# Kernel tuning notes

Measured on AMD Instinct MI355X. Metric: run time of the kernel, lower is better.

Reference implementation:

```python
import jax, jax.numpy as jnp
import numpy as np

N_NODES = 100000
N_EDGES = 1600000
D_IN = 128
D_HID = 128
D_OUT = 2
BN_EPS = 1e-5


def _sage_conv(x, src, dst, W_l, b_l, W_r):
    # PyG SAGEConv (aggr='mean'): out = lin_l(mean_{j in N(i)} x_j) + lin_r(x_i)
    # messages flow src -> dst
    agg = jax.ops.segment_sum(x[src], dst, num_segments=x.shape[0])
    deg = jax.ops.segment_sum(jnp.ones((src.shape[0],), x.dtype), dst,
                              num_segments=x.shape[0])
    mean = agg / jnp.maximum(deg, 1.0)[:, None]
    return mean @ W_l + b_l + x @ W_r


def _batch_norm(x, gamma, beta):
    # training-mode BatchNorm1d math over the node dimension (biased var)
    mu = jnp.mean(x, axis=0)
    var = jnp.var(x, axis=0)
    return (x - mu) * jax.lax.rsqrt(var + BN_EPS) * gamma + beta


def setup_inputs() -> dict:
    key = jax.random.key(0)
    ks = jax.random.split(key, 10)
    s = lambda d: 1.0 / np.sqrt(d)
    x = jax.random.normal(ks[0], (N_NODES, D_IN), dtype=jnp.float32)
    edge_index = jax.random.randint(ks[1], (2, N_EDGES), 0, N_NODES, dtype=jnp.int64)
    W1l = jax.random.uniform(ks[2], (D_IN, D_HID), jnp.float32, -s(D_IN), s(D_IN))
    b1 = jax.random.uniform(ks[3], (D_HID,), jnp.float32, -s(D_IN), s(D_IN))
    W1r = jax.random.uniform(ks[4], (D_IN, D_HID), jnp.float32, -s(D_IN), s(D_IN))
    W2l = jax.random.uniform(ks[5], (D_HID, D_OUT), jnp.float32, -s(D_HID), s(D_HID))
    b2 = jax.random.uniform(ks[6], (D_OUT,), jnp.float32, -s(D_HID), s(D_HID))
    W2r = jax.random.uniform(ks[7], (D_HID, D_OUT), jnp.float32, -s(D_HID), s(D_HID))
    gamma1 = jnp.ones((D_HID,), jnp.float32)
    beta1 = jnp.zeros((D_HID,), jnp.float32)
    gamma2 = jnp.ones((D_OUT,), jnp.float32)
    beta2 = jnp.zeros((D_OUT,), jnp.float32)
    return {"x": x, "edge_index": edge_index,
            "W1l": W1l, "b1": b1, "W1r": W1r, "gamma1": gamma1, "beta1": beta1,
            "W2l": W2l, "b2": b2, "W2r": W2r, "gamma2": gamma2, "beta2": beta2}


def reference(x, edge_index, W1l, b1, W1r, gamma1, beta1,
              W2l, b2, W2r, gamma2, beta2):
    src, dst = edge_index[0], edge_index[1]
    h = _sage_conv(x, src, dst, W1l, b1, W1r)
    h = _batch_norm(h, gamma1, beta1)
    h = jax.nn.relu(h)
    # dropout in eval mode = identity
    h = _sage_conv(h, src, dst, W2l, b2, W2r)
    h = _batch_norm(h, gamma2, beta2)
    return jax.nn.log_softmax(h, axis=1)
```

## Files before the change

### kernel.cpp

```cpp
#include <hip/hip_runtime.h>
#include <hip/hip_bf16.h>
#include <math.h>


#define DH 128
#define PAD 64
#define NPB 128
#define CAPB (NPB * PAD)
#define MAXBINS 1024
#define MAXCHUNK 6400
#define SENT 0xFFFFFFFFu
#define L1BLOCKS 512

typedef short short8 __attribute__((ext_vector_type(8)));
typedef float float4v __attribute__((ext_vector_type(4)));
typedef float float2v __attribute__((ext_vector_type(2)));
typedef unsigned uint4v __attribute__((ext_vector_type(4)));

template <typename T> static __device__ __forceinline__ float tof(T v);
template <> __device__ __forceinline__ float tof<float>(float v) { return v; }
template <> __device__ __forceinline__ float tof<__hip_bfloat16>(__hip_bfloat16 v) {
  return __bfloat162float(v);
}

static __device__ __forceinline__ short f2bf_s(float f) {
  union { __hip_bfloat16 h; short s; } u;
  u.h = __float2bfloat16(f);
  return u.s;
}

static __device__ __forceinline__ float bf2f(short s) {
  union { unsigned u; float f; } c;
  c.u = ((unsigned)(unsigned short)s) << 16;
  return c.f;
}

static __device__ __forceinline__ float asf(unsigned u) {
  union { unsigned u; float f; } c;
  c.u = u;
  return c.f;
}

__global__ void k_probe(const unsigned* __restrict__ xw,
                        const unsigned* __restrict__ ew,
                        int* __restrict__ flags) {
  int t = threadIdx.x;
  unsigned wx = xw[(size_t)t * 23456 + 7];
  unsigned el = (wx >> 7) & 0xFFu;
  int sx = (el >= 0x60 && el <= 0x85) ? 1 : 0;
  unsigned we = ew[(size_t)t * 12000 + 1];
  int se = (we == 0) ? 1 : 0;
  __shared__ int c[2];
  if (t < 2) c[t] = 0;
  __syncthreads();
  atomicAdd(&c[0], sx);
  atomicAdd(&c[1], se);
  __syncthreads();
  if (t == 0) {
    flags[0] = (c[0] < 192) ? 1 : 0;
    flags[2] = (c[1] > 192) ? 1 : 0;
  }
}

template <typename FT>
static __device__ __forceinline__ void wt_one(const FT* __restrict__ W1l,
                                              const FT* __restrict__ W1r,
                                              short* __restrict__ WT, int idx) {
  int n = idx >> 8, k = idx & 255;
  float v = (k < 128) ? tof(W1l[k * 128 + n]) : tof(W1r[(k - 128) * 128 + n]);
  WT[n * 256 + (k ^ ((n & 7) << 3))] = f2bf_s(v);
}
__global__ void k_xbwt(const void* __restrict__ x, const void* __restrict__ W1l,
                       const void* __restrict__ W1r, const int* __restrict__ flags,
                       __hip_bfloat162* __restrict__ xb, short* __restrict__ WT,
                       int total2) {
  int gi = blockIdx.x * blockDim.x + threadIdx.x;
  bool f32 = flags[0] != 0;
  if (gi < 32768) {
    if (f32) wt_one<float>((const float*)W1l, (const float*)W1r, WT, gi);
    else wt_one<__hip_bfloat16>((const __hip_bfloat16*)W1l, (const __hip_bfloat16*)W1r, WT, gi);
  }
  int i = gi - 32768;
  if (i >= 0 && i < total2) {
    if (f32) {
      float2 v = ((const float2*)x)[i];
      __hip_bfloat162 o;
      o.x = __float2bfloat16(v.x);
      o.y = __float2bfloat16(v.y);
      xb[i] = o;
    } else {
      xb[i] = ((const __hip_bfloat162*)x)[i];
    }
  }
}

template <typename IT>
static __device__ __forceinline__ void binscatter_agg_body(
    const IT* __restrict__ es, const IT* __restrict__ ed,
    int* __restrict__ binCnt, unsigned* __restrict__ pairs,
    int E, int N, int chunk, int NB) {
  __shared__ int cnt[MAXBINS];
  __shared__ int sc[MAXBINS];
  __shared__ int gbase[MAXBINS];
  __shared__ unsigned buf[MAXCHUNK];
  int t = threadIdx.x;
  int e0 = blockIdx.x * chunk;
  int e1 = min(e0 + chunk, E);
  int nE = e1 - e0;
  if (nE <= 0) return;

  for (int b = t; b < MAXBINS; b += 256) cnt[b] = 0;
  __syncthreads();
  for (int i = t; i < nE; i += 256) {
    int d = (int)ed[e0 + i];
    if ((unsigned)d >= (unsigned)N) d = 0;
    atomicAdd(&cnt[d >> 7], 1);
  }
  __syncthreads();
  for (int b = t; b < MAXBINS; b += 256) sc[b] = cnt[b];
  __syncthreads();
  for (int off = 1; off < MAXBINS; off <<= 1) {
    int v[MAXBINS / 256];
#pragma unroll
    for (int j = 0; j < MAXBINS / 256; ++j) {
      int b = t + j * 256;
      v[j] = (b >= off) ? sc[b - off] : 0;
    }
    __syncthreads();
#pragma unroll
    for (int j = 0; j < MAXBINS / 256; ++j) sc[t + j * 256] += v[j];
    __syncthreads();
  }
  for (int b = t; b < NB; b += 256) {
    int c = cnt[b];
    sc[b] -= c;
    int g = 0;
    if (c > 0) g = atomicAdd(&binCnt[b * 16], c);
    gbase[b] = g;
    cnt[b] = 0;
  }
  __syncthreads();
  for (int i = t; i < nE; i += 256) {
    int s = (int)es[e0 + i], d = (int)ed[e0 + i];
    if ((unsigned)s >= (unsigned)N) s = 0;
    if ((unsigned)d >= (unsigned)N) d = 0;
    int bin = d >> 7;
    int p = atomicAdd(&cnt[bin], 1);
    buf[sc[bin] + p] = ((unsigned)(d & (NPB - 1)) << 20) | (unsigned)s;
  }
  __syncthreads();
  for (int b = t; b < NB; b += 256) {
    int c = cnt[b];
    if (c == 0) continue;
    int g = gbase[b];
    if (g >= CAPB) continue;
    int cv = min(c, CAPB - g);
    unsigned* dst = pairs + (size_t)b * CAPB + g;
    const unsigned* srcp = buf + sc[b];
    for (int j = 0; j < cv; ++j) dst[j] = srcp[j];
  }
}
__launch_bounds__(256)
__global__ void k_binscatter_agg(const void* __restrict__ ev, const int* __restrict__ flags,
                                 int* __restrict__ binCnt, unsigned* __restrict__ pairs,
                                 int E, int N, int chunk, int NB) {
  if (flags[2]) binscatter_agg_body<long long>((const long long*)ev, (const long long*)ev + E,
                                               binCnt, pairs, E, N, chunk, NB);
  else          binscatter_agg_body<int>((const int*)ev, (const int*)ev + E,
                                         binCnt, pairs, E, N, chunk, NB);
}

__launch_bounds__(256)
__global__ void k_binbuild(const unsigned* __restrict__ pairs,
                           const int* __restrict__ binCnt,
                           int* __restrict__ deg_i, int* __restrict__ srcs_pad, int N) {
  __shared__ int cnt[NPB];
  __shared__ int lst[NPB * PAD];
  int bin = blockIdx.x;
  int t = threadIdx.x;
  for (int i = t; i < NPB; i += 256) cnt[i] = 0;
  for (int i = t; i < NPB * PAD; i += 256) lst[i] = 0;
  __syncthreads();
  int m = min(binCnt[bin * 16], CAPB);
  const unsigned* pp = pairs + (size_t)bin * CAPB;
  for (int i = t; i < m; i += 256) {
    unsigned u = pp[i];
    if (u == SENT) continue;
    int local = u >> 20;
    int s = u & 0xFFFFF;
    int r = atomicAdd(&cnt[local], 1);
    if (r < PAD) lst[local * PAD + r] = s;
  }
  __syncthreads();
  int base = bin * NPB;
  for (int i = t; i < NPB; i += 256) {
    int node = base + i;
    if (node < N) deg_i[node] = cnt[i];
  }
  for (int i = t; i < NPB * PAD; i += 256) {
    int node = base + (i >> 6);
    if (node < N) srcs_pad[(size_t)base * PAD + i] = lst[i];
  }
}

static __device__ __forceinline__ void accum8(float2v acc[4], uint4v u) {
#pragma unroll
  for (int i = 0; i < 4; ++i) {
    float2v p;
    p[0] = asf(u[i] << 16);
    p[1] = asf(u[i] & 0xFFFF0000u);
    acc[i] += p;
  }
}
static __device__ __forceinline__ uint4v maskv(uint4v v, int keep) {
  unsigned m = keep ? 0xFFFFFFFFu : 0u;
  uint4v r;
#pragma unroll
  for (int i = 0; i < 4; ++i) r[i] = v[i] & m;
  return r;
}
__launch_bounds__(256)
__global__ void k_gather(const unsigned* __restrict__ xbu,
                         const int* __restrict__ deg_i, const int* __restrict__ srcs_pad,
                         short* __restrict__ meanbs, int N) {
  int node = blockIdx.x * 4 + (threadIdx.x >> 6);
  int lane = threadIdx.x & 63;
  int g = lane >> 4, l = lane & 15;
  if (node >= N) return;
  int dg = deg_i[node];
  int cnt = min(dg, PAD);
  const int* sl = srcs_pad + (size_t)node * PAD;
  int srcv = sl[lane];
  const uint4v* xv = (const uint4v*)xbu;
  float2v acc[4];
#pragma unroll
  for (int i = 0; i < 4; ++i) acc[i] = (float2v){0.f, 0.f};

  if (cnt > 0) {
    int sA0 = __shfl(srcv, g);
    int sA1 = __shfl(srcv, 4 + g);
    int sA2 = __shfl(srcv, 8 + g);
    int sA3 = __shfl(srcv, 12 + g);
    uint4v a0 = xv[(size_t)sA0 * 16 + l];
    uint4v a1 = xv[(size_t)sA1 * 16 + l];
    uint4v a2 = xv[(size_t)sA2 * 16 + l];
    uint4v a3 = xv[(size_t)sA3 * 16 + l];
    uint4v b0, b1, b2, b3;
    bool hb = cnt > 16;
    if (hb) {
      int sB0 = __shfl(srcv, 16 + g);
      int sB1 = __shfl(srcv, 20 + g);
      int sB2 = __shfl(srcv, 24 + g);
      int sB3 = __shfl(srcv, 28 + g);
      b0 = xv[(size_t)sB0 * 16 + l];
      b1 = xv[(size_t)sB1 * 16 + l];
      b2 = xv[(size_t)sB2 * 16 + l];
      b3 = xv[(size_t)sB3 * 16 + l];
    }
    a0 = maskv(a0, g < cnt);
    a1 = maskv(a1, 4 + g < cnt);
    a2 = maskv(a2, 8 + g < cnt);
    a3 = maskv(a3, 12 + g < cnt);
    accum8(acc, a0);
    accum8(acc, a1);
    accum8(acc, a2);
    accum8(acc, a3);
    if (hb) {
      b0 = maskv(b0, 16 + g < cnt);
      b1 = maskv(b1, 20 + g < cnt);
      b2 = maskv(b2, 24 + g < cnt);
      b3 = maskv(b3, 28 + g < cnt);
      accum8(acc, b0);
      accum8(acc, b1);
      accum8(acc, b2);
      accum8(acc, b3);
    }
    for (int j = 32; j < cnt; j += 16) {
      int s0 = __shfl(srcv, j + g);
      int s1 = __shfl(srcv, j + 4 + g);
      int s2 = __shfl(srcv, j + 8 + g);
      int s3 = __shfl(srcv, j + 12 + g);
      uint4v v0 = xv[(size_t)s0 * 16 + l];
      uint4v v1 = xv[(size_t)s1 * 16 + l];
      uint4v v2 = xv[(size_t)s2 * 16 + l];
      uint4v v3 = xv[(size_t)s3 * 16 + l];
      v0 = maskv(v0, j + g < cnt);
      v1 = maskv(v1, j + 4 + g < cnt);
      v2 = maskv(v2, j + 8 + g < cnt);
      v3 = maskv(v3, j + 12 + g < cnt);
      accum8(acc, v0);
      accum8(acc, v1);
      accum8(acc, v2);
      accum8(acc, v3);
    }
  }

#pragma unroll
  for (int i = 0; i < 4; ++i) {
#pragma unroll
    for (int c = 0; c < 2; ++c) {
      acc[i][c] += __shfl_xor(acc[i][c], 16);
      acc[i][c] += __shfl_xor(acc[i][c], 32);
    }
  }
  if (g == 0) {
    float invd = 1.0f / fmaxf((float)dg, 1.0f);
    short8 o;
#pragma unroll
    for (int i = 0; i < 4; ++i) {
      o[2 * i]     = f2bf_s(acc[i][0] * invd);
      o[2 * i + 1] = f2bf_s(acc[i][1] * invd);
    }
    *(short8*)(meanbs + (size_t)node * DH + l * 8) = o;
  }
}

template <typename FT>
static __device__ __forceinline__ void layer1_body(
    const short* __restrict__ meanbs, const short* __restrict__ xbs,
    const short* __restrict__ WTs, const FT* __restrict__ b1,
    __hip_bfloat16* __restrict__ h1, float* __restrict__ st1,
    int N, int ntiles) {
  __shared__ short ldsWT[32768];
  int t = threadIdx.x;
  {
    const uint4v* src = (const uint4v*)WTs;
    uint4v* dst = (uint4v*)ldsWT;
#pragma unroll
    for (int i = 0; i < 16; ++i) dst[t + i * 256] = src[t + i * 256];
  }
  __syncthreads();

  int w = t >> 6;
  int lane = t & 63;
  int m = lane & 15;
  int quad = lane >> 4;
  int xm = (m & 7) << 3;

  float bs[8], bq[8];
#pragma unroll
  for (int c = 0; c < 8; ++c) { bs[c] = 0.f; bq[c] = 0.f; }
  float bias[8];
#pragma unroll
  for (int c = 0; c < 8; ++c) bias[c] = tof(b1[c * 16 + m]);

  for (int tt = blockIdx.x; tt < ntiles; tt += gridDim.x) {
    int rowbase = tt * 64 + w * 16;
    int arowc = min(rowbase + m, N - 1);

    short8 afrag[8];
    const short* mr = meanbs + (size_t)arowc * DH;
#pragma unroll
    for (int kt = 0; kt < 4; ++kt)
      afrag[kt] = *(const short8*)(mr + kt * 32 + quad * 8);
    const short* xr = xbs + (size_t)arowc * DH;
#pragma unroll
    for (int kt = 0; kt < 4; ++kt)
      afrag[4 + kt] = *(const short8*)(xr + kt * 32 + quad * 8);

    float4v acc[8];
#pragma unroll
    for (int c = 0; c < 8; ++c) acc[c] = (float4v){0.f, 0.f, 0.f, 0.f};

#pragma unroll
    for (int kt = 0; kt < 8; ++kt) {
      int koff = (kt * 32 + quad * 8) ^ xm;
#pragma unroll
      for (int c = 0; c < 8; ++c) {
        short8 b = *(const short8*)(ldsWT + (c * 16 + m) * 256 + koff);
        acc[c] = __builtin_amdgcn_mfma_f32_16x16x32_bf16(afrag[kt], b, acc[c], 0, 0, 0);
      }
    }

#pragma unroll
    for (int c = 0; c < 8; ++c) {
      int col = c * 16 + m;
#pragma unroll
      for (int r = 0; r < 4; ++r) {
        int ro = rowbase + quad * 4 + r;
        float v = acc[c][r] + bias[c];
        if (ro < N) {
          h1[(size_t)ro * DH + col] = __float2bfloat16(v);
          bs[c] += v;
          bq[c] += v * v;
        }
      }
    }
  }

  __syncthreads();
  float* lsum = (float*)ldsWT;
  float* lsq  = lsum + 512;
#pragma unroll
  for (int c = 0; c < 8; ++c) {
    float s = bs[c], q = bq[c];
    s += __shfl_xor(s, 16); s += __shfl_xor(s, 32);
    q += __shfl_xor(q, 16); q += __shfl_xor(q, 32);
    if (quad == 0) { lsum[w * 128 + c * 16 + m] = s; lsq[w * 128 + c * 16 + m] = q; }
  }
  __syncthreads();
  if (t < 128) {
    float s = lsum[0 * 128 + t] + lsum[1 * 128 + t] + lsum[2 * 128 + t] + lsum[3 * 128 + t];
    float q = lsq[0 * 128 + t] + lsq[1 * 128 + t] + lsq[2 * 128 + t] + lsq[3 * 128 + t];
    unsafeAtomicAdd(&st1[t], s);
    unsafeAtomicAdd(&st1[128 + t], q);
  }
}
__launch_bounds__(256)
__global__ void k_layer1(const short* __restrict__ meanbs, const short* __restrict__ xbs,
                         const short* __restrict__ WTs, const void* __restrict__ b1,
                         const int* __restrict__ flags,
                         __hip_bfloat16* __restrict__ h1, float* __restrict__ st1,
                         int N, int ntiles) {
  if (flags[0])
    layer1_body<float>(meanbs, xbs, WTs, (const float*)b1, h1, st1, N, ntiles);
  else
    layer1_body<__hip_bfloat16>(meanbs, xbs, WTs, (const __hip_bfloat16*)b1,
                                h1, st1, N, ntiles);
}

template <typename FT>
static __device__ __forceinline__ void zr_body(
    const short* __restrict__ h1s, const float* __restrict__ stats1,
    const FT* __restrict__ g1, const FT* __restrict__ be1,
    const FT* __restrict__ W2l, const FT* __restrict__ W2r,
    float4* __restrict__ zr, int N) {
  __shared__ float sc[128], sh[128];
  int t = threadIdx.x;
  if (t < 128) {
    float invN = 1.0f / (float)N;
    float mu = stats1[t] * invN;
    float var = stats1[128 + t] * invN - mu * mu;
    float a = tof(g1[t]) * rsqrtf(var + 1e-5f);
    sc[t] = a;
    sh[t] = tof(be1[t]) - mu * a;
  }
  __syncthreads();
  int lane = t & 63, w = t >> 6;
  int g = lane >> 4, l = lane & 15;
  int f0 = l * 8;
  float scl[8], shl[8], wl0[8], wl1[8], wr0[8], wr1[8];
#pragma unroll
  for (int j = 0; j < 8; ++j) {
    int f = f0 + j;
    scl[j] = sc[f];
    shl[j] = sh[f];
    wl0[j] = tof(W2l[f * 2 + 0]);
    wl1[j] = tof(W2l[f * 2 + 1]);
    wr0[j] = tof(W2r[f * 2 + 0]);
    wr1[j] = tof(W2r[f * 2 + 1]);
  }
  int gw = blockIdx.x * 4 + w;
  int nw = gridDim.x * 4;
  for (int base = gw * 4; base < N; base += nw * 4) {
    int node = base + g;
    if (node < N) {
      short8 hv = *(const short8*)(h1s + (size_t)node * DH + f0);
      float z0 = 0.f, z1 = 0.f, r0 = 0.f, r1 = 0.f;
#pragma unroll
      for (int j = 0; j < 8; ++j) {
        float v = fmaxf(bf2f(hv[j]) * scl[j] + shl[j], 0.0f);
        z0 += v * wl0[j];
        z1 += v * wl1[j];
        r0 += v * wr0[j];
        r1 += v * wr1[j];
      }
#pragma unroll
      for (int off = 8; off >= 1; off >>= 1) {
        z0 += __shfl_xor(z0, off);
        z1 += __shfl_xor(z1, off);
        r0 += __shfl_xor(r0, off);
        r1 += __shfl_xor(r1, off);
      }
      if (l == 0) zr[node] = make_float4(z0, z1, r0, r1);
    }
  }
}
__launch_bounds__(256)
__global__ void k_zr(const __hip_bfloat16* __restrict__ h1, const float* __restrict__ st1,
                     const void* g1, const void* be1, const void* W2l, const void* W2r,
                     const int* __restrict__ flags, float4* __restrict__ zr, int N) {
  if (flags[0])
    zr_body<float>((const short*)h1, st1, (const float*)g1, (const float*)be1,
                   (const float*)W2l, (const float*)W2r, zr, N);
  else
    zr_body<__hip_bfloat16>((const short*)h1, st1, (const __hip_bfloat16*)g1,
                            (const __hip_bfloat16*)be1,
                            (const __hip_bfloat16*)W2l, (const __hip_bfloat16*)W2r, zr, N);
}

template <typename FT>
static __device__ __forceinline__ void h2_body(
    const float2* __restrict__ z2, const int* __restrict__ deg_i,
    const int* __restrict__ srcs_pad, const FT* __restrict__ b2,
    float2* __restrict__ h2, float* __restrict__ stats2, int N) {
  int lane = threadIdx.x & 63, w = threadIdx.x >> 6;
  int g = lane >> 4, l = lane & 15;
  float bs0 = 0.f, bs1 = 0.f, bq0 = 0.f, bq1 = 0.f;
  float bb0 = tof(b2[0]), bb1 = tof(b2[1]);
  int gw = blockIdx.x * 4 + w;
  int nw = gridDim.x * 4;
  for (int base = gw * 4; base < N; base += nw * 4) {
    int node = base + g;
    float za = 0.f, zb = 0.f;
    int dg_true = 0;
    if (node < N) {
      dg_true = deg_i[node];
      int cnt = min(dg_true, PAD);
      const int* sl = srcs_pad + (size_t)node * PAD;
      for (int j = l; j < cnt; j += 16) {
        float2 v = z2[2 * sl[j]];
        za += v.x;
        zb += v.y;
      }
    }
#pragma unroll
    for (int off = 8; off >= 1; off >>= 1) {
      za += __shfl_xor(za, off);
      zb += __shfl_xor(zb, off);
    }
    if (node < N && l == 0) {
      float dg = fmaxf((float)dg_true, 1.0f);
      float2 rw = z2[2 * node + 1];
      float h0 = za / dg + rw.x + bb0;
      float h1v = zb / dg + rw.y + bb1;
      h2[node] = make_float2(h0, h1v);
      bs0 += h0; bs1 += h1v; bq0 += h0 * h0; bq1 += h1v * h1v;
    }
  }
  bs0 += __shfl_xor(bs0, 16); bs0 += __shfl_xor(bs0, 32);
  bs1 += __shfl_xor(bs1, 16); bs1 += __shfl_xor(bs1, 32);
  bq0 += __shfl_xor(bq0, 16); bq0 += __shfl_xor(bq0, 32);
  bq1 += __shfl_xor(bq1, 16); bq1 += __shfl_xor(bq1, 32);
  __shared__ float red[4][4];
  if (lane == 0) { red[w][0] = bs0; red[w][1] = bs1; red[w][2] = bq0; red[w][3] = bq1; }
  __syncthreads();
  if (threadIdx.x < 4) {
    float a = red[0][threadIdx.x] + red[1][threadIdx.x] +
              red[2][threadIdx.x] + red[3][threadIdx.x];
    unsafeAtomicAdd(&stats2[threadIdx.x], a);
  }
}
__launch_bounds__(256)
__global__ void k_h2(const float4* __restrict__ zr, const int* __restrict__ deg_i,
                     const int* __restrict__ srcs_pad, const void* b2,
                     const int* __restrict__ flags,
                     float2* __restrict__ h2, float* __restrict__ stats2, int N) {
  if (flags[0])
    h2_body<float>((const float2*)zr, deg_i, srcs_pad, (const float*)b2, h2, stats2, N);
  else
    h2_body<__hip_bfloat16>((const float2*)zr, deg_i, srcs_pad,
                            (const __hip_bfloat16*)b2, h2, stats2, N);
}

template <typename FT>
static __device__ __forceinline__ void out_body(
    const float2* __restrict__ h2, const float* __restrict__ stats2,
    const FT* __restrict__ g2, const FT* __restrict__ be2,
    void* __restrict__ out, int N) {
  int i = blockIdx.x * blockDim.x + threadIdx.x;
  if (i >= N) return;
  float invN = 1.0f / (float)N;
  float mu0 = stats2[0] * invN, mu1 = stats2[1] * invN;
  float v0 = stats2[2] * invN - mu0 * mu0;
  float v1 = stats2[3] * invN - mu1 * mu1;
  float r0 = rsqrtf(v0 + 1e-5f), r1 = rsqrtf(v1 + 1e-5f);
  float2 h = h2[i];
  float y0 = (h.x - mu0) * r0 * tof(g2[0]) + tof(be2[0]);
  float y1 = (h.y - mu1) * r1 * tof(g2[1]) + tof(be2[1]);
  float mx = fmaxf(y0, y1);
  float lse = mx + logf(expf(y0 - mx) + expf(y1 - mx));
  float o0 = y0 - lse, o1 = y1 - lse;
  if (sizeof(FT) == 4) {
    ((float2*)out)[i] = make_float2(o0, o1);
  } else {
    __hip_bfloat162 o;
    o.x = __float2bfloat16(o0);
    o.y = __float2bfloat16(o1);
    ((__hip_bfloat162*)out)[i] = o;
  }
}
__global__ void k_out(const float2* __restrict__ h2, const float* __restrict__ stats2,
                      const void* g2, const void* be2, const int* __restrict__ flags,
                      void* __restrict__ out, int N) {
  if (flags[0]) out_body<float>(h2, stats2, (const float*)g2, (const float*)be2, out, N);
  else out_body<__hip_bfloat16>(h2, stats2, (const __hip_bfloat16*)g2,
                                (const __hip_bfloat16*)be2, out, N);
}

extern "C" void kernel_launch(void* const* d_in, const int* in_sizes, int n_in,
                              void* d_out, int out_size, void* d_ws, size_t ws_size,
                              hipStream_t stream) {
  int ix = 0, ie = 1, iW1l = 2, ib1 = 3, iW1r = 4, ig1 = 5, ibe1 = 6,
      iW2l = 7, ib2 = 8, iW2r = 9, ig2 = 10, ibe2 = 11;
  if (n_in == 12) {
    int best = -1, second = -1;
    for (int i = 0; i < 12; ++i) {
      if (best < 0 || in_sizes[i] > in_sizes[best]) { second = best; best = i; }
      else if (second < 0 || in_sizes[i] > in_sizes[second]) second = i;
    }
    ix = best; ie = second;
    int c16384 = 0, c128 = 0, c256 = 0, c2 = 0;
    for (int i = 0; i < 12; ++i) {
      if (i == ix || i == ie) continue;
      int s = in_sizes[i];
      if (s == 16384) { if (c16384++ == 0) iW1l = i; else iW1r = i; }
      else if (s == 128) { if (c128 == 0) ib1 = i; else if (c128 == 1) ig1 = i; else ibe1 = i; c128++; }
      else if (s == 256) { if (c256++ == 0) iW2l = i; else iW2r = i; }
      else { if (c2 == 0) ib2 = i; else if (c2 == 1) ig2 = i; else ibe2 = i; c2++; }
    }
  }

  const void* x   = d_in[ix];
  const void* ev  = d_in[ie];
  const void* W1l = d_in[iW1l];
  const void* b1  = d_in[ib1];
  const void* W1r = d_in[iW1r];
  const void* g1  = d_in[ig1];
  const void* be1 = d_in[ibe1];
  const void* W2l = d_in[iW2l];
  const void* b2  = d_in[ib2];
  const void* W2r = d_in[iW2r];
  const void* g2  = d_in[ig2];
  const void* be2 = d_in[ibe2];

  int N = in_sizes[ix] / DH;
  int E = in_sizes[ie] / 2;
  int nb = (N + 63) / 64;
  int NB = (N + NPB - 1) / NPB;

  int nblk = 1024;
  if ((E + nblk - 1) / nblk > MAXCHUNK) nblk = (E + MAXCHUNK - 1) / MAXCHUNK;
  int chunk = (E + nblk - 1) / nblk;

  int grid1 = (nb < L1BLOCKS) ? nb : L1BLOCKS;

  char* ws = (char*)d_ws;
  size_t off = 0;
  auto alloc = [&](size_t b) { size_t o = off; off += (b + 255) & ~(size_t)255; return o; };
  size_t o_st1   = alloc(256 * 4);
  size_t o_st2   = alloc(4 * 4);
  size_t o_bcnt  = alloc((size_t)NB * 16 * 4);
  size_t zlen = off;
  size_t o_pairs = alloc((size_t)NB * CAPB * 4);
  size_t o_degi  = alloc((size_t)N * 4);
  size_t o_srcs  = alloc((size_t)N * PAD * 4);
  size_t o_xb    = alloc((size_t)N * DH * 2);
  size_t o_mean  = alloc((size_t)N * DH * 2);
  size_t o_h1    = alloc((size_t)N * DH * 2);
  size_t o_wt    = alloc(256 * 128 * 2);
  size_t o_zr    = alloc((size_t)N * 16);
  size_t o_h2    = alloc((size_t)N * 8);
  size_t o_flg   = alloc(64);

  float* st1  = (float*)(ws + o_st1);
  float* st2  = (float*)(ws + o_st2);
  int* bcnt   = (int*)(ws + o_bcnt);
  unsigned* pairs = (unsigned*)(ws + o_pairs);
  int* deg_i  = (int*)(ws + o_degi);
  int* srcs   = (int*)(ws + o_srcs);
  __hip_bfloat162* xb = (__hip_bfloat162*)(ws + o_xb);
  short* meanb = (short*)(ws + o_mean);
  __hip_bfloat16* h1 = (__hip_bfloat16*)(ws + o_h1);
  short* WT   = (short*)(ws + o_wt);
  float4* zrp = (float4*)(ws + o_zr);
  float2* h2p = (float2*)(ws + o_h2);
  int* flags  = (int*)(ws + o_flg);

  hipMemsetAsync(d_ws, 0, zlen, stream);

  int total2 = N * 64;
  k_probe<<<1, 256, 0, stream>>>((const unsigned*)x, (const unsigned*)ev, flags);
  k_xbwt<<<(total2 + 32768 + 255) / 256, 256, 0, stream>>>(x, W1l, W1r, flags, xb, WT, total2);
  k_binscatter_agg<<<nblk, 256, 0, stream>>>(ev, flags, bcnt, pairs, E, N, chunk, NB);
  k_binbuild<<<NB, 256, 0, stream>>>(pairs, bcnt, deg_i, srcs, N);
  k_gather<<<(N + 3) / 4, 256, 0, stream>>>((const unsigned*)xb, deg_i, srcs, meanb, N);
  k_layer1<<<grid1, 256, 0, stream>>>(meanb, (const short*)xb, WT, b1,
                                      flags, h1, st1, N, nb);
  k_zr<<<2048, 256, 0, stream>>>(h1, st1, g1, be1, W2l, W2r, flags, zrp, N);
  k_h2<<<2048, 256, 0, stream>>>(zrp, deg_i, srcs, b2, flags, h2p, st2, N);
  k_out<<<(N + 255) / 256, 256, 0, stream>>>(h2p, st2, g2, be2, flags, d_out, N);
}
```

Measured before the change: 334.7 us.

## Replace two-pass binned adjacency build with direct global-atomic scatter

Removes the two-kernel bin scatter plus per-bin local build and replaces it with a single grid-stride kernel that atomically increments per-node degree in global memory and writes each source directly into its padded slot. This drops the intermediate pairs buffer and one launch, but swaps shared-memory atomics and coalesced writes for 1.6M scattered global atomics and scattered stores. Unused padded slots are no longer zero-filled, so the gather now clamps any out-of-range source index to stay in bounds.

New measurement: 389.8 us. 1.16x slower.

```diff
diff --git a/kernel.cpp b/kernel.cpp
--- a/kernel.cpp
+++ b/kernel.cpp
@@ -5,11 +5,6 @@
 
 #define DH 128
 #define PAD 64
-#define NPB 128
-#define CAPB (NPB * PAD)
-#define MAXBINS 1024
-#define MAXCHUNK 6400
-#define SENT 0xFFFFFFFFu
 #define L1BLOCKS 512
 
 typedef short short8 __attribute__((ext_vector_type(8)));
@@ -95,112 +90,26 @@
 }
 
 template <typename IT>
-static __device__ __forceinline__ void binscatter_agg_body(
+static __device__ __forceinline__ void edges_body(
     const IT* __restrict__ es, const IT* __restrict__ ed,
-    int* __restrict__ binCnt, unsigned* __restrict__ pairs,
-    int E, int N, int chunk, int NB) {
-  __shared__ int cnt[MAXBINS];
-  __shared__ int sc[MAXBINS];
-  __shared__ int gbase[MAXBINS];
-  __shared__ unsigned buf[MAXCHUNK];
-  int t = threadIdx.x;
-  int e0 = blockIdx.x * chunk;
-  int e1 = min(e0 + chunk, E);
-  int nE = e1 - e0;
-  if (nE <= 0) return;
-
-  for (int b = t; b < MAXBINS; b += 256) cnt[b] = 0;
-  __syncthreads();
-  for (int i = t; i < nE; i += 256) {
-    int d = (int)ed[e0 + i];
-    if ((unsigned)d >= (unsigned)N) d = 0;
-    atomicAdd(&cnt[d >> 7], 1);
-  }
-  __syncthreads();
-  for (int b = t; b < MAXBINS; b += 256) sc[b] = cnt[b];
-  __syncthreads();
-  for (int off = 1; off < MAXBINS; off <<= 1) {
-    int v[MAXBINS / 256];
-#pragma unroll
-    for (int j = 0; j < MAXBINS / 256; ++j) {
-      int b = t + j * 256;
-      v[j] = (b >= off) ? sc[b - off] : 0;
-    }
-    __syncthreads();
-#pragma unroll
-    for (int j = 0; j < MAXBINS / 256; ++j) sc[t + j * 256] += v[j];
-    __syncthreads();
-  }
-  for (int b = t; b < NB; b += 256) {
-    int c = cnt[b];
-    sc[b] -= c;
-    int g = 0;
-    if (c > 0) g = atomicAdd(&binCnt[b * 16], c);
-    gbase[b] = g;
-    cnt[b] = 0;
-  }
-  __syncthreads();
-  for (int i = t; i < nE; i += 256) {
-    int s = (int)es[e0 + i], d = (int)ed[e0 + i];
+    int* __restrict__ deg_i, int* __restrict__ srcs_pad, int E, int N) {
+  int stride = gridDim.x * blockDim.x;
+  for (int i = blockIdx.x * blockDim.x + threadIdx.x; i < E; i += stride) {
+    int s = (int)es[i], d = (int)ed[i];
     if ((unsigned)s >= (unsigned)N) s = 0;
     if ((unsigned)d >= (unsigned)N) d = 0;
-    int bin = d >> 7;
-    int p = atomicAdd(&cnt[bin], 1);
-    buf[sc[bin] + p] = ((unsigned)(d & (NPB - 1)) << 20) | (unsigned)s;
-  }
-  __syncthreads();
-  for (int b = t; b < NB; b += 256) {
-    int c = cnt[b];
-    if (c == 0) continue;
-    int g = gbase[b];
-    if (g >= CAPB) continue;
-    int cv = min(c, CAPB - g);
-    unsigned* dst = pairs + (size_t)b * CAPB + g;
-    const unsigned* srcp = buf + sc[b];
-    for (int j = 0; j < cv; ++j) dst[j] = srcp[j];
+    int r = atomicAdd(&deg_i[d], 1);
+    if (r < PAD) srcs_pad[(size_t)d * PAD + r] = s;
   }
 }
 __launch_bounds__(256)
-__global__ void k_binscatter_agg(const void* __restrict__ ev, const int* __restrict__ flags,
-                                 int* __restrict__ binCnt, unsigned* __restrict__ pairs,
-                                 int E, int N, int chunk, int NB) {
-  if (flags[2]) binscatter_agg_body<long long>((const long long*)ev, (const long long*)ev + E,
-                                               binCnt, pairs, E, N, chunk, NB);
-  else          binscatter_agg_body<int>((const int*)ev, (const int*)ev + E,
-                                         binCnt, pairs, E, N, chunk, NB);
-}
-
-__launch_bounds__(256)
-__global__ void k_binbuild(const unsigned* __restrict__ pairs,
-                           const int* __restrict__ binCnt,
-                           int* __restrict__ deg_i, int* __restrict__ srcs_pad, int N) {
-  __shared__ int cnt[NPB];
-  __shared__ int lst[NPB * PAD];
-  int bin = blockIdx.x;
-  int t = threadIdx.x;
-  for (int i = t; i < NPB; i += 256) cnt[i] = 0;
-  for (int i = t; i < NPB * PAD; i += 256) lst[i] = 0;
-  __syncthreads();
-  int m = min(binCnt[bin * 16], CAPB);
-  const unsigned* pp = pairs + (size_t)bin * CAPB;
-  for (int i = t; i < m; i += 256) {
-    unsigned u = pp[i];
-    if (u == SENT) continue;
-    int local = u >> 20;
-    int s = u & 0xFFFFF;
-    int r = atomicAdd(&cnt[local], 1);
-    if (r < PAD) lst[local * PAD + r] = s;
-  }
-  __syncthreads();
-  int base = bin * NPB;
-  for (int i = t; i < NPB; i += 256) {
-    int node = base + i;
-    if (node < N) deg_i[node] = cnt[i];
-  }
-  for (int i = t; i < NPB * PAD; i += 256) {
-    int node = base + (i >> 6);
-    if (node < N) srcs_pad[(size_t)base * PAD + i] = lst[i];
-  }
+__global__ void k_edges(const void* __restrict__ ev, const int* __restrict__ flags,
+                        int* __restrict__ deg_i, int* __restrict__ srcs_pad,
+                        int E, int N) {
+  if (flags[2]) edges_body<long long>((const long long*)ev, (const long long*)ev + E,
+                                      deg_i, srcs_pad, E, N);
+  else          edges_body<int>((const int*)ev, (const int*)ev + E,
+                                deg_i, srcs_pad, E, N);
 }
 
 static __device__ __forceinline__ void accum8(float2v acc[4], uint4v u) {
@@ -231,6 +140,7 @@
   int cnt = min(dg, PAD);
   const int* sl = srcs_pad + (size_t)node * PAD;
   int srcv = sl[lane];
+  srcv = ((unsigned)srcv < (unsigned)N) ? srcv : 0;
   const uint4v* xv = (const uint4v*)xbu;
   float2v acc[4];
 #pragma unroll
@@ -627,11 +537,6 @@
   int N = in_sizes[ix] / DH;
   int E = in_sizes[ie] / 2;
   int nb = (N + 63) / 64;
-  int NB = (N + NPB - 1) / NPB;
-
-  int nblk = 1024;
-  if ((E + nblk - 1) / nblk > MAXCHUNK) nblk = (E + MAXCHUNK - 1) / MAXCHUNK;
-  int chunk = (E + nblk - 1) / nblk;
 
   int grid1 = (nb < L1BLOCKS) ? nb : L1BLOCKS;
 
@@ -640,10 +545,8 @@
   auto alloc = [&](size_t b) { size_t o = off; off += (b + 255) & ~(size_t)255; return o; };
   size_t o_st1   = alloc(256 * 4);
   size_t o_st2   = alloc(4 * 4);
-  size_t o_bcnt  = alloc((size_t)NB * 16 * 4);
+  size_t o_degi  = alloc((size_t)N * 4);
   size_t zlen = off;
-  size_t o_pairs = alloc((size_t)NB * CAPB * 4);
-  size_t o_degi  = alloc((size_t)N * 4);
   size_t o_srcs  = alloc((size_t)N * PAD * 4);
   size_t o_xb    = alloc((size_t)N * DH * 2);
   size_t o_mean  = alloc((size_t)N * DH * 2);
@@ -655,8 +558,6 @@
 
   float* st1  = (float*)(ws + o_st1);
   float* st2  = (float*)(ws + o_st2);
-  int* bcnt   = (int*)(ws + o_bcnt);
-  unsigned* pairs = (unsigned*)(ws + o_pairs);
   int* deg_i  = (int*)(ws + o_degi);
   int* srcs   = (int*)(ws + o_srcs);
   __hip_bfloat162* xb = (__hip_bfloat162*)(ws + o_xb);
@@ -672,8 +573,7 @@
   int total2 = N * 64;
   k_probe<<<1, 256, 0, stream>>>((const unsigned*)x, (const unsigned*)ev, flags);
   k_xbwt<<<(total2 + 32768 + 255) / 256, 256, 0, stream>>>(x, W1l, W1r, flags, xb, WT, total2);
-  k_binscatter_agg<<<nblk, 256, 0, stream>>>(ev, flags, bcnt, pairs, E, N, chunk, NB);
-  k_binbuild<<<NB, 256, 0, stream>>>(pairs, bcnt, deg_i, srcs, N);
+  k_edges<<<2048, 256, 0, stream>>>(ev, flags, deg_i, srcs, E, N);
   k_gather<<<(N + 3) / 4, 256, 0, stream>>>((const unsigned*)xb, deg_i, srcs, meanb, N);
   k_layer1<<<grid1, 256, 0, stream>>>(meanb, (const short*)xb, WT, b1,
                                       flags, h1, st1, N, nb);
```
